# Kernel tuning notes

Hardware: AMD Instinct MI355X
Metric: run time of the kernel (lower is better)

The kernel has to match this reference:

```python
import jax, jax.numpy as jnp
import numpy as np
import math

M = 8                      # multiplicity (channels per irrep)
COMBOS = [(0,0,0),(0,1,1),(1,0,1),(1,1,0),(1,1,1),(2,1,1)]  # (edge_l, node_l, out_l)

def _cg_coeff(j1, m1, j2, m2, j3, m3):
    # standard (Racah) complex Clebsch-Gordan coefficient <j1 m1 j2 m2 | j3 m3>
    if m3 != m1 + m2:
        return 0.0
    f = math.factorial
    vmin = max(0, j2 - j3 - m1, j1 + m2 - j3)
    vmax = min(j1 + j2 - j3, j1 - m1, j2 + m2)
    pref = (2*j3 + 1) * f(j3+j1-j2) * f(j3-j1+j2) * f(j1+j2-j3) / f(j1+j2+j3+1)
    pref *= f(j3+m3) * f(j3-m3) * f(j1-m1) * f(j1+m1) * f(j2-m2) * f(j2+m2)
    s = 0.0
    for v in range(vmin, vmax + 1):
        s += (-1)**v / (f(v) * f(j1+j2-j3-v) * f(j1-m1-v) * f(j2+m2-v)
                        * f(j3-j2+m1+v) * f(j3-j1-m2+v))
    return math.sqrt(pref) * s

def _su2_cg(l1, l2, l3):
    C = np.zeros((2*l1+1, 2*l2+1, 2*l3+1), dtype=np.complex128)
    for m1 in range(-l1, l1+1):
        for m2 in range(-l2, l2+1):
            m3 = m1 + m2
            if -l3 <= m3 <= l3:
                C[m1+l1, m2+l2, m3+l3] = _cg_coeff(l1, m1, l2, m2, l3, m3)
    return C

def _qmat(l):
    # real -> complex spherical-harmonic change of basis (e3nn convention)
    q = np.zeros((2*l+1, 2*l+1), dtype=np.complex128)
    for m in range(-l, 0):
        q[l+m, l+abs(m)] = 1/np.sqrt(2)
        q[l+m, l-abs(m)] = -1j/np.sqrt(2)
    q[l, l] = 1.0
    for m in range(1, l+1):
        q[l+m, l+abs(m)] = (-1)**m / np.sqrt(2)
        q[l+m, l-abs(m)] = 1j * (-1)**m / np.sqrt(2)
    return (-1j)**l * q

def _so3_cg(l1, l2, l3):
    # real-basis CG, normalized to unit Frobenius norm (matches e3nn _so3_clebsch_gordan)
    C = np.einsum('ij,kl,mn,ikn->jlm', _qmat(l1), _qmat(l2),
                  np.conj(_qmat(l3)).T, _su2_cg(l1, l2, l3))
    assert np.abs(C.imag).max() < 1e-6
    C = C.real
    return C / np.linalg.norm(C)

CG = {c: jnp.asarray(_so3_cg(*c), dtype=jnp.float32) for c in COMBOS}


def setup_inputs() -> dict:
    N, E = 100000, 1600000
    ks = jax.random.split(jax.random.key(0), 6)
    return {
        'node_irreps': jax.random.normal(ks[0], (N, 4*M), jnp.float32),
        'edge_index': jax.random.randint(ks[1], (2, E), 0, N, dtype=jnp.int32),
        'sh0': jax.random.normal(ks[2], (E, 1), jnp.float32),
        'sh1': jax.random.normal(ks[3], (E, 3), jnp.float32),
        'sh2': jax.random.normal(ks[4], (E, 5), jnp.float32),
        'W': jax.random.normal(ks[5], (len(COMBOS), M, M), jnp.float32),
    }


def reference(node_irreps, edge_index, sh0, sh1, sh2, W):
    N, E = node_irreps.shape[0], edge_index.shape[1]
    src = node_irreps[edge_index[0]]                    # gather: [E, 4M]
    feats = {0: src[:, :M][:, :, None],                 # scalar channels [E, M, 1]
             1: src[:, M:].reshape(E, M, 3)}            # vector channels [E, M, 3]
    sh = {0: sh0, 1: sh1, 2: sh2}
    msg = {0: jnp.zeros((E, M, 1), node_irreps.dtype),
           1: jnp.zeros((E, M, 3), node_irreps.dtype)}
    for idx, (le, ln, lo) in enumerate(COMBOS):
        # per-edge CG tensor product: [de,dn,do] x [E,de] x [E,M,dn] -> [E,M,do]
        base = jnp.einsum('ijk,ei,emj->emk', CG[(le, ln, lo)], sh[le], feats[ln])
        # channel-mixing scalar weights (in_channel -> out_channel)
        msg[lo] = msg[lo] + jnp.einsum('io,eik->eok', W[idx], base)
    tgt = edge_index[1]
    agg0 = jax.ops.segment_sum(msg[0].reshape(E, M), tgt, num_segments=N)     # [N, M]
    agg1 = jax.ops.segment_sum(msg[1].reshape(E, 3*M), tgt, num_segments=N)   # [N, 3M]
    return jnp.concatenate([agg0, agg1], axis=1)
```

## Files before the change

### kernel.cpp

```cpp
#include <hip/hip_runtime.h>

#define THREADS 256


__global__ __launch_bounds__(THREADS) void k_hist2(const int* __restrict__ tgt,
                                                   int* __restrict__ cnt,
                                                   int* __restrict__ ke, int E) {
    int e = blockIdx.x * THREADS + threadIdx.x;
    if (e < E) ke[e] = atomicAdd(&cnt[tgt[e]], 1);
}

__global__ __launch_bounds__(THREADS) void k_scan_partial(const int* __restrict__ cnt,
                                                          int* __restrict__ bsum, int N) {
    __shared__ int lds[THREADS];
    int base = blockIdx.x * 1024 + threadIdx.x * 4;
    int s = 0;
    #pragma unroll
    for (int k = 0; k < 4; ++k) { int i = base + k; if (i < N) s += cnt[i]; }
    lds[threadIdx.x] = s; __syncthreads();
    for (int off = THREADS / 2; off > 0; off >>= 1) {
        if (threadIdx.x < off) lds[threadIdx.x] += lds[threadIdx.x + off];
        __syncthreads();
    }
    if (threadIdx.x == 0) bsum[blockIdx.x] = lds[0];
}

__global__ __launch_bounds__(1024) void k_scan_bsum(int* __restrict__ bsum, int NB) {
    __shared__ int lds[1024];
    int t = threadIdx.x;
    int v = (t < NB) ? bsum[t] : 0;
    lds[t] = v; __syncthreads();
    for (int off = 1; off < 1024; off <<= 1) {
        int x = (t >= off) ? lds[t - off] : 0;
        __syncthreads();
        lds[t] += x;
        __syncthreads();
    }
    if (t < NB) bsum[t] = lds[t] - v;
}

__global__ __launch_bounds__(THREADS) void k_scan_final(int* __restrict__ cnt,
                                                        const int* __restrict__ bsum,
                                                        int* __restrict__ rowptr,
                                                        int N, int E) {
    __shared__ int lds[THREADS];
    int base = blockIdx.x * 1024 + threadIdx.x * 4;
    int v[4]; int local = 0;
    #pragma unroll
    for (int k = 0; k < 4; ++k) {
        int i = base + k;
        v[k] = (i < N) ? cnt[i] : 0;
        local += v[k];
    }
    lds[threadIdx.x] = local; __syncthreads();
    for (int off = 1; off < THREADS; off <<= 1) {
        int x = (threadIdx.x >= off) ? lds[threadIdx.x - off] : 0;
        __syncthreads();
        lds[threadIdx.x] += x;
        __syncthreads();
    }
    int p = lds[threadIdx.x] - local + bsum[blockIdx.x];
    #pragma unroll
    for (int k = 0; k < 4; ++k) {
        int i = base + k;
        if (i < N) { rowptr[i] = p; p += v[k]; }
    }
    if (blockIdx.x == 0 && threadIdx.x == 0) rowptr[N] = E;
}


__global__ __launch_bounds__(THREADS) void k_scatter(const int* __restrict__ eidx,
                                                     const int* __restrict__ ke,
                                                     const int* __restrict__ rowptr,
                                                     const float* __restrict__ sh0,
                                                     const float* __restrict__ sh1,
                                                     const float* __restrict__ sh2,
                                                     float* __restrict__ payload,
                                                     int E) {
    int e = blockIdx.x * THREADS + threadIdx.x;
    if (e >= E) return;
    int src = eidx[e];
    int tgt = eidx[E + e];
    int pos = rowptr[tgt] + ke[e];

    float4 p0 = make_float4(sh0[e], sh1[3*e+0], sh1[3*e+1], sh1[3*e+2]);
    float4 p1 = make_float4(sh2[5*e+0], sh2[5*e+1], sh2[5*e+2], sh2[5*e+3]);
    float4 p2 = make_float4(sh2[5*e+4], __int_as_float(src), 0.f, 0.f);
    float4 p3 = make_float4(0.f, 0.f, 0.f, 0.f);

    float4* pr = (float4*)(payload + (size_t)pos * 16);
    pr[0] = p0; pr[1] = p1; pr[2] = p2; pr[3] = p3;
}


__global__ __launch_bounds__(THREADS) void k_agg2(const float* __restrict__ node,
                                                  const int*   __restrict__ rowptr,
                                                  const float* __restrict__ payload,
                                                  const float* __restrict__ W,
                                                  float*       __restrict__ out, int N) {
    __shared__ float sW[384];
    __shared__ float sAcc[32 * 8 * 14];
    for (int t = threadIdx.x; t < 384; t += THREADS) sW[t] = W[t];
    __syncthreads();

    constexpr float IS3  = 0.57735026918962576f;
    constexpr float IS6  = 0.40824829046386302f;
    constexpr float IS10 = 0.31622776601683794f;
    constexpr float IS30 = 0.18257418583505536f;

    const int nodeSlot = threadIdx.x >> 3;
    const int i        = threadIdx.x & 7;
    const int n        = blockIdx.x * 32 + nodeSlot;

    float a[14];
    #pragma unroll
    for (int k = 0; k < 14; ++k) a[k] = 0.f;

    if (n < N) {
        const int jbeg = rowptr[n];
        const int jend = rowptr[n + 1];
        for (int j = jbeg; j < jend; ++j) {
            const float4* pr = (const float4*)(payload + (size_t)j * 16);
            const float4 p0 = pr[0];
            const float4 p1 = pr[1];
            const float4 p2 = pr[2];
            const int src = __float_as_int(p2.y);

            const float* nr = node + (size_t)src * 32;
            const float f0 = nr[i];
            const float x  = nr[8 + 3*i + 0];
            const float y  = nr[8 + 3*i + 1];
            const float z  = nr[8 + 3*i + 2];

            const float s  = p0.x, u0 = p0.y, u1 = p0.z, u2 = p0.w;
            const float q0 = p1.x, q1 = p1.y, q2 = p1.z, q3 = p1.w, q4 = p2.x;

            const float Q00 = -q2*IS30 - q4*IS10;
            const float Q01 =  q1*IS10;
            const float Q02 =  q0*IS10;
            const float Q11 =  2.0f*q2*IS30;
            const float Q12 =  q3*IS10;
            const float Q22 = -q2*IS30 + q4*IS10;

            a[0]  += s * f0;
            a[1]  += u0*x + u1*y + u2*z;
            a[2]  += s * x;
            a[3]  += s * y;
            a[4]  += s * z;
            a[5]  += f0 * u0;
            a[6]  += f0 * u1;
            a[7]  += f0 * u2;
            a[8]  += u1*z - u2*y;
            a[9]  += u2*x - u0*z;
            a[10] += u0*y - u1*x;
            a[11] += Q00*x + Q01*y + Q02*z;
            a[12] += Q01*x + Q11*y + Q12*z;
            a[13] += Q02*x + Q12*y + Q22*z;
        }
    }

    #pragma unroll
    for (int k = 1; k < 8; ++k) a[k] *= IS3;
    #pragma unroll
    for (int k = 8; k < 11; ++k) a[k] *= IS6;

    float* myAcc = &sAcc[(nodeSlot * 8 + i) * 14];
    #pragma unroll
    for (int k = 0; k < 14; ++k) myAcc[k] = a[k];
    __syncthreads();

    if (n < N) {
        const int o = i;
        float o0 = 0.f, ox = 0.f, oy = 0.f, oz = 0.f;
        #pragma unroll
        for (int ii = 0; ii < 8; ++ii) {
            const float* A = &sAcc[(nodeSlot * 8 + ii) * 14];
            const float w0 = sW[  0 + ii*8 + o];
            const float w1 = sW[ 64 + ii*8 + o];
            const float w2 = sW[128 + ii*8 + o];
            const float w3 = sW[192 + ii*8 + o];
            const float w4 = sW[256 + ii*8 + o];
            const float w5 = sW[320 + ii*8 + o];
            o0 += w0*A[0]  + w3*A[1];
            ox += w1*A[2]  + w2*A[5] + w4*A[8]  + w5*A[11];
            oy += w1*A[3]  + w2*A[6] + w4*A[9]  + w5*A[12];
            oz += w1*A[4]  + w2*A[7] + w4*A[10] + w5*A[13];
        }
        float* orow = out + (size_t)n * 32;
        orow[o]         = o0;
        orow[8 + 3*o+0] = ox;
        orow[8 + 3*o+1] = oy;
        orow[8 + 3*o+2] = oz;
    }
}


__global__ __launch_bounds__(THREADS) void msg_kernel_atomic(
    const float* __restrict__ node,
    const int*   __restrict__ eidx,
    const float* __restrict__ sh0,
    const float* __restrict__ sh1,
    const float* __restrict__ sh2,
    const float* __restrict__ W,
    float*       __restrict__ out,
    int E)
{
    __shared__ float sW[384];
    for (int t = threadIdx.x; t < 384; t += THREADS) sW[t] = W[t];
    __syncthreads();

    int e = blockIdx.x * THREADS + threadIdx.x;
    if (e >= E) return;

    constexpr float IS3  = 0.57735026918962576f;
    constexpr float IS6  = 0.40824829046386302f;
    constexpr float IS10 = 0.31622776601683794f;
    constexpr float IS30 = 0.18257418583505536f;

    const int src = eidx[e];
    const int tgt = eidx[E + e];

    const float s  = sh0[e];
    const float u0 = sh1[3*e+0], u1 = sh1[3*e+1], u2 = sh1[3*e+2];
    const float q0 = sh2[5*e+0], q1 = sh2[5*e+1], q2 = sh2[5*e+2],
                q3 = sh2[5*e+3], q4 = sh2[5*e+4];

    const float Q00 = -q2*IS30 - q4*IS10;
    const float Q01 =  q1*IS10;
    const float Q02 =  q0*IS10;
    const float Q11 =  2.0f*q2*IS30;
    const float Q12 =  q3*IS10;
    const float Q22 = -q2*IS30 + q4*IS10;

    float f[32];
    {
        const float4* nr = (const float4*)(node + (size_t)src * 32);
        #pragma unroll
        for (int i = 0; i < 8; ++i) {
            float4 v = nr[i];
            f[4*i+0]=v.x; f[4*i+1]=v.y; f[4*i+2]=v.z; f[4*i+3]=v.w;
        }
    }

    float msg[32];
    #pragma unroll
    for (int j = 0; j < 32; ++j) msg[j] = 0.0f;

    const float s13 = s * IS3;

    #pragma unroll
    for (int i = 0; i < 8; ++i) {
        const float f0i = f[i];
        const float x = f[8+3*i+0], y = f[8+3*i+1], z = f[8+3*i+2];
        const float c0  = s * f0i;
        const float c3  = IS3 * (u0*x + u1*y + u2*z);
        const float p2  = IS3 * f0i;
        const float c1x = s13*x, c1y = s13*y, c1z = s13*z;
        const float c2x = p2*u0, c2y = p2*u1, c2z = p2*u2;
        const float c4x = IS6*(u1*z - u2*y);
        const float c4y = IS6*(u2*x - u0*z);
        const float c4z = IS6*(u0*y - u1*x);
        const float c5x = Q00*x + Q01*y + Q02*z;
        const float c5y = Q01*x + Q11*y + Q12*z;
        const float c5z = Q02*x + Q12*y + Q22*z;

        float wr[6][8];
        #pragma unroll
        for (int c = 0; c < 6; ++c) {
            float4 aa = *(const float4*)&sW[c*64 + i*8 + 0];
            float4 bb = *(const float4*)&sW[c*64 + i*8 + 4];
            wr[c][0]=aa.x; wr[c][1]=aa.y; wr[c][2]=aa.z; wr[c][3]=aa.w;
            wr[c][4]=bb.x; wr[c][5]=bb.y; wr[c][6]=bb.z; wr[c][7]=bb.w;
        }

        #pragma unroll
        for (int o = 0; o < 8; ++o) {
            msg[o] += wr[0][o]*c0 + wr[3][o]*c3;
            msg[8+3*o+0] += wr[1][o]*c1x + wr[2][o]*c2x + wr[4][o]*c4x + wr[5][o]*c5x;
            msg[8+3*o+1] += wr[1][o]*c1y + wr[2][o]*c2y + wr[4][o]*c4y + wr[5][o]*c5y;
            msg[8+3*o+2] += wr[1][o]*c1z + wr[2][o]*c2z + wr[4][o]*c4z + wr[5][o]*c5z;
        }
    }

    float* orow = out + (size_t)tgt * 32;
    #pragma unroll
    for (int j = 0; j < 32; ++j) unsafeAtomicAdd(orow + j, msg[j]);
}


extern "C" void kernel_launch(void* const* d_in, const int* in_sizes, int n_in,
                              void* d_out, int out_size, void* d_ws, size_t ws_size,
                              hipStream_t stream) {
    const float* node = (const float*)d_in[0];
    const int*   eidx = (const int*)d_in[1];
    const float* sh0  = (const float*)d_in[2];
    const float* sh1  = (const float*)d_in[3];
    const float* sh2  = (const float*)d_in[4];
    const float* W    = (const float*)d_in[5];
    float* out = (float*)d_out;

    const int E = in_sizes[2];
    const int N = in_sizes[0] / 32;
    const int NB = (N + 1023) / 1024;

    size_t int_words = (size_t)(N + 1) + N + 1024 + (size_t)E;
    size_t pay_off_w = (int_words + 15) & ~(size_t)15;
    size_t need      = (pay_off_w + (size_t)E * 16) * sizeof(float);

    if (ws_size >= need && NB <= 1024) {
        int* rowptr = (int*)d_ws;
        int* cnt    = rowptr + (N + 1);
        int* bsum   = cnt + N;
        int* ke     = bsum + 1024;
        float* payload = (float*)d_ws + pay_off_w;

        hipMemsetAsync(cnt, 0, (size_t)N * sizeof(int), stream);

        k_hist2<<<(E + THREADS - 1) / THREADS, THREADS, 0, stream>>>(eidx + E, cnt, ke, E);
        k_scan_partial<<<NB, THREADS, 0, stream>>>(cnt, bsum, N);
        k_scan_bsum<<<1, 1024, 0, stream>>>(bsum, NB);
        k_scan_final<<<NB, THREADS, 0, stream>>>(cnt, bsum, rowptr, N, E);
        k_scatter<<<(E + THREADS - 1) / THREADS, THREADS, 0, stream>>>(
            eidx, ke, rowptr, sh0, sh1, sh2, payload, E);

        k_agg2<<<(N + 31) / 32, THREADS, 0, stream>>>(node, rowptr, payload, W, out, N);
    } else {
        hipMemsetAsync(d_out, 0, (size_t)out_size * sizeof(float), stream);
        msg_kernel_atomic<<<(E + THREADS - 1) / THREADS, THREADS, 0, stream>>>(
            node, eidx, sh0, sh1, sh2, W, out, E);
    }
}
```

Baseline: 355.2 us.

## Use atomic cursors in scatter, drop per-edge rank array, prefetch payload in aggregation

```diff
diff --git a/kernel.cpp b/kernel.cpp
--- a/kernel.cpp
+++ b/kernel.cpp
@@ -3,11 +3,10 @@
 #define THREADS 256
 
 
-__global__ __launch_bounds__(THREADS) void k_hist2(const int* __restrict__ tgt,
-                                                   int* __restrict__ cnt,
-                                                   int* __restrict__ ke, int E) {
+__global__ __launch_bounds__(THREADS) void k_hist(const int* __restrict__ tgt,
+                                                  int* __restrict__ cnt, int E) {
     int e = blockIdx.x * THREADS + threadIdx.x;
-    if (e < E) ke[e] = atomicAdd(&cnt[tgt[e]], 1);
+    if (e < E) atomicAdd(&cnt[tgt[e]], 1);
 }
 
 __global__ __launch_bounds__(THREADS) void k_scan_partial(const int* __restrict__ cnt,
@@ -39,9 +38,10 @@
     if (t < NB) bsum[t] = lds[t] - v;
 }
 
-__global__ __launch_bounds__(THREADS) void k_scan_final(int* __restrict__ cnt,
+__global__ __launch_bounds__(THREADS) void k_scan_final(const int* __restrict__ cnt,
                                                         const int* __restrict__ bsum,
                                                         int* __restrict__ rowptr,
+                                                        int* __restrict__ cursor,
                                                         int N, int E) {
     __shared__ int lds[THREADS];
     int base = blockIdx.x * 1024 + threadIdx.x * 4;
@@ -63,15 +63,14 @@
     #pragma unroll
     for (int k = 0; k < 4; ++k) {
         int i = base + k;
-        if (i < N) { rowptr[i] = p; p += v[k]; }
+        if (i < N) { rowptr[i] = p; cursor[i] = p; p += v[k]; }
     }
     if (blockIdx.x == 0 && threadIdx.x == 0) rowptr[N] = E;
 }
 
 
 __global__ __launch_bounds__(THREADS) void k_scatter(const int* __restrict__ eidx,
-                                                     const int* __restrict__ ke,
-                                                     const int* __restrict__ rowptr,
+                                                     int* __restrict__ cursor,
                                                      const float* __restrict__ sh0,
                                                      const float* __restrict__ sh1,
                                                      const float* __restrict__ sh2,
@@ -81,17 +80,21 @@
     if (e >= E) return;
     int src = eidx[e];
     int tgt = eidx[E + e];
-    int pos = rowptr[tgt] + ke[e];
 
     float4 p0 = make_float4(sh0[e], sh1[3*e+0], sh1[3*e+1], sh1[3*e+2]);
     float4 p1 = make_float4(sh2[5*e+0], sh2[5*e+1], sh2[5*e+2], sh2[5*e+3]);
-    float4 p2 = make_float4(sh2[5*e+4], __int_as_float(src), 0.f, 0.f);
-    float4 p3 = make_float4(0.f, 0.f, 0.f, 0.f);
-
-    float4* pr = (float4*)(payload + (size_t)pos * 16);
-    pr[0] = p0; pr[1] = p1; pr[2] = p2; pr[3] = p3;
-}
-
+    float2 p2 = make_float2(sh2[5*e+4], __int_as_float(src));
+
+    int pos = atomicAdd(&cursor[tgt], 1);
+
+    float* pr = payload + (size_t)pos * 16;
+    *(float4*)(pr + 0) = p0;
+    *(float4*)(pr + 4) = p1;
+    *(float2*)(pr + 8) = p2;
+}
+
+
+#define ACC_STRIDE 15
 
 __global__ __launch_bounds__(THREADS) void k_agg2(const float* __restrict__ node,
                                                   const int*   __restrict__ rowptr,
@@ -99,7 +102,7 @@
                                                   const float* __restrict__ W,
                                                   float*       __restrict__ out, int N) {
     __shared__ float sW[384];
-    __shared__ float sAcc[32 * 8 * 14];
+    __shared__ float sAcc[32 * 8 * ACC_STRIDE];
     for (int t = threadIdx.x; t < 384; t += THREADS) sW[t] = W[t];
     __syncthreads();
 
@@ -119,43 +122,56 @@
     if (n < N) {
         const int jbeg = rowptr[n];
         const int jend = rowptr[n + 1];
-        for (int j = jbeg; j < jend; ++j) {
-            const float4* pr = (const float4*)(payload + (size_t)j * 16);
-            const float4 p0 = pr[0];
-            const float4 p1 = pr[1];
-            const float4 p2 = pr[2];
-            const int src = __float_as_int(p2.y);
-
-            const float* nr = node + (size_t)src * 32;
-            const float f0 = nr[i];
-            const float x  = nr[8 + 3*i + 0];
-            const float y  = nr[8 + 3*i + 1];
-            const float z  = nr[8 + 3*i + 2];
-
-            const float s  = p0.x, u0 = p0.y, u1 = p0.z, u2 = p0.w;
-            const float q0 = p1.x, q1 = p1.y, q2 = p1.z, q3 = p1.w, q4 = p2.x;
-
-            const float Q00 = -q2*IS30 - q4*IS10;
-            const float Q01 =  q1*IS10;
-            const float Q02 =  q0*IS10;
-            const float Q11 =  2.0f*q2*IS30;
-            const float Q12 =  q3*IS10;
-            const float Q22 = -q2*IS30 + q4*IS10;
-
-            a[0]  += s * f0;
-            a[1]  += u0*x + u1*y + u2*z;
-            a[2]  += s * x;
-            a[3]  += s * y;
-            a[4]  += s * z;
-            a[5]  += f0 * u0;
-            a[6]  += f0 * u1;
-            a[7]  += f0 * u2;
-            a[8]  += u1*z - u2*y;
-            a[9]  += u2*x - u0*z;
-            a[10] += u0*y - u1*x;
-            a[11] += Q00*x + Q01*y + Q02*z;
-            a[12] += Q01*x + Q11*y + Q12*z;
-            a[13] += Q02*x + Q12*y + Q22*z;
+
+        if (jbeg < jend) {
+            const float* pr = payload + (size_t)jbeg * 16;
+            float4 c0 = *(const float4*)(pr + 0);
+            float4 c1 = *(const float4*)(pr + 4);
+            float2 c2 = *(const float2*)(pr + 8);
+
+            for (int j = jbeg; j < jend; ++j) {
+                float4 n0, n1; float2 n2;
+                if (j + 1 < jend) {
+                    const float* prn = payload + (size_t)(j + 1) * 16;
+                    n0 = *(const float4*)(prn + 0);
+                    n1 = *(const float4*)(prn + 4);
+                    n2 = *(const float2*)(prn + 8);
+                }
+
+                const int src = __float_as_int(c2.y);
+                const float* nr = node + (size_t)src * 32;
+                const float f0 = nr[i];
+                const float x  = nr[8 + 3*i + 0];
+                const float y  = nr[8 + 3*i + 1];
+                const float z  = nr[8 + 3*i + 2];
+
+                const float s  = c0.x, u0 = c0.y, u1 = c0.z, u2 = c0.w;
+                const float q0 = c1.x, q1 = c1.y, q2 = c1.z, q3 = c1.w, q4 = c2.x;
+
+                const float Q00 = -q2*IS30 - q4*IS10;
+                const float Q01 =  q1*IS10;
+                const float Q02 =  q0*IS10;
+                const float Q11 =  2.0f*q2*IS30;
+                const float Q12 =  q3*IS10;
+                const float Q22 = -q2*IS30 + q4*IS10;
+
+                a[0]  += s * f0;
+                a[1]  += u0*x + u1*y + u2*z;
+                a[2]  += s * x;
+                a[3]  += s * y;
+                a[4]  += s * z;
+                a[5]  += f0 * u0;
+                a[6]  += f0 * u1;
+                a[7]  += f0 * u2;
+                a[8]  += u1*z - u2*y;
+                a[9]  += u2*x - u0*z;
+                a[10] += u0*y - u1*x;
+                a[11] += Q00*x + Q01*y + Q02*z;
+                a[12] += Q01*x + Q11*y + Q12*z;
+                a[13] += Q02*x + Q12*y + Q22*z;
+
+                c0 = n0; c1 = n1; c2 = n2;
+            }
         }
     }
 
@@ -164,7 +180,7 @@
     #pragma unroll
     for (int k = 8; k < 11; ++k) a[k] *= IS6;
 
-    float* myAcc = &sAcc[(nodeSlot * 8 + i) * 14];
+    float* myAcc = &sAcc[(nodeSlot * 8 + i) * ACC_STRIDE];
     #pragma unroll
     for (int k = 0; k < 14; ++k) myAcc[k] = a[k];
     __syncthreads();
@@ -174,7 +190,7 @@
         float o0 = 0.f, ox = 0.f, oy = 0.f, oz = 0.f;
         #pragma unroll
         for (int ii = 0; ii < 8; ++ii) {
-            const float* A = &sAcc[(nodeSlot * 8 + ii) * 14];
+            const float* A = &sAcc[(nodeSlot * 8 + ii) * ACC_STRIDE];
             const float w0 = sW[  0 + ii*8 + o];
             const float w1 = sW[ 64 + ii*8 + o];
             const float w2 = sW[128 + ii*8 + o];
@@ -303,25 +319,25 @@
     const int N = in_sizes[0] / 32;
     const int NB = (N + 1023) / 1024;
 
-    size_t int_words = (size_t)(N + 1) + N + 1024 + (size_t)E;
+    size_t int_words = (size_t)(N + 1) + N + N + 1024;
     size_t pay_off_w = (int_words + 15) & ~(size_t)15;
     size_t need      = (pay_off_w + (size_t)E * 16) * sizeof(float);
 
     if (ws_size >= need && NB <= 1024) {
         int* rowptr = (int*)d_ws;
-        int* cnt    = rowptr + (N + 1);
+        int* cursor = rowptr + (N + 1);
+        int* cnt    = cursor + N;
         int* bsum   = cnt + N;
-        int* ke     = bsum + 1024;
         float* payload = (float*)d_ws + pay_off_w;
 
         hipMemsetAsync(cnt, 0, (size_t)N * sizeof(int), stream);
 
-        k_hist2<<<(E + THREADS - 1) / THREADS, THREADS, 0, stream>>>(eidx + E, cnt, ke, E);
+        k_hist<<<(E + THREADS - 1) / THREADS, THREADS, 0, stream>>>(eidx + E, cnt, E);
         k_scan_partial<<<NB, THREADS, 0, stream>>>(cnt, bsum, N);
         k_scan_bsum<<<1, 1024, 0, stream>>>(bsum, NB);
-        k_scan_final<<<NB, THREADS, 0, stream>>>(cnt, bsum, rowptr, N, E);
+        k_scan_final<<<NB, THREADS, 0, stream>>>(cnt, bsum, rowptr, cursor, N, E);
         k_scatter<<<(E + THREADS - 1) / THREADS, THREADS, 0, stream>>>(
-            eidx, ke, rowptr, sh0, sh1, sh2, payload, E);
+            eidx, cursor, sh0, sh1, sh2, payload, E);
 
         k_agg2<<<(N + 31) / 32, THREADS, 0, stream>>>(node, rowptr, payload, W, out, N);
     } else {
```

New measurement: 351.0 us. About the same (-1.2%).
